# Optimization experiments

Measured on AMD Instinct MI355X. Metric: run time of the kernel, lower is better.

Reference implementation:

```python
import jax, jax.numpy as jnp
import numpy as np

N = 50000      # nodes
E = 500000     # edges
IN = 128       # in_channels
HID = 64       # hidden_channels
OUT = 128      # out_channels
H = 4          # heads
NEG_SLOPE = 0.2


def _glorot(key, shape):
    fan_in, fan_out = shape[0], shape[-1]
    lim = np.sqrt(6.0 / (fan_in + fan_out))
    return jax.random.uniform(key, shape, jnp.float32, -lim, lim)


def setup_inputs() -> dict:
    key = jax.random.key(0)
    ks = jax.random.split(key, 12)
    return {
        "x": jax.random.normal(ks[0], (N, IN), jnp.float32),
        "edge_index": jax.random.randint(ks[1], (2, E), 0, N, jnp.int64),
        "edge_weight": jax.random.uniform(ks[2], (E,), jnp.float32),
        # layer 1: IN -> H*HID
        "W1": _glorot(ks[3], (IN, H * HID)),
        "b1": jnp.zeros((H * HID,), jnp.float32),
        "att1": _glorot(ks[4], (H, HID)),
        # layer 2: HID -> H*HID  (update() means over heads -> HID features)
        "W2": _glorot(ks[5], (HID, H * HID)),
        "b2": jnp.zeros((H * HID,), jnp.float32),
        "att2": _glorot(ks[6], (H, HID)),
        # layer 3: HID -> H*OUT
        "W3": _glorot(ks[7], (HID, H * OUT)),
        "b3": jnp.zeros((H * OUT,), jnp.float32),
        "att3": _glorot(ks[8], (H, OUT)),
    }


def _gat_layer(x, W, b, att, src, dst, edge_weight, out_dim):
    # lin + reshape to [N, H, D]
    h = (x @ W + b).reshape(-1, H, out_dim)
    xj = h[src]                                   # gather source feats [E,H,D]
    alpha = jnp.sum(xj * att[None], axis=-1)      # per-edge att score [E,H]
    alpha = jax.nn.leaky_relu(alpha, NEG_SLOPE)
    alpha = alpha * edge_weight[:, None]
    alpha = jax.nn.softmax(alpha, axis=1)         # softmax over HEADS (dim=1, as in source)
    msg = xj * alpha[:, :, None]                  # [E,H,D]
    aggr = jax.ops.segment_sum(msg, dst, num_segments=N)  # scatter-add [N,H,D]
    return aggr.mean(axis=1)                      # update(): mean over heads -> [N,D]


def reference(x, edge_index, edge_weight, W1, b1, att1, W2, b2, att2, W3, b3, att3):
    src, dst = edge_index[0], edge_index[1]
    h = _gat_layer(x, W1, b1, att1, src, dst, edge_weight, HID)
    h = jax.nn.relu(h)
    h = _gat_layer(h, W2, b2, att2, src, dst, edge_weight, HID)
    h = jax.nn.relu(h)
    return _gat_layer(h, W3, b3, att3, src, dst, edge_weight, OUT)
```

## Files before the change

kernel.cpp:

```cpp
#include <hip/hip_runtime.h>
#include <hip/hip_bf16.h>

#define NHEAD 4
#define NEG 0.2f

typedef __bf16 bf16x8 __attribute__((ext_vector_type(8)));
typedef __bf16 bf16x4 __attribute__((ext_vector_type(4)));
typedef float f32x4 __attribute__((ext_vector_type(4)));

__device__ __forceinline__ float blo(unsigned u) { return __uint_as_float(u << 16); }
__device__ __forceinline__ float bhi(unsigned u) { return __uint_as_float(u & 0xffff0000u); }
__device__ __forceinline__ unsigned short fbits(float f) {
    __bf16 h = (__bf16)f;
    return *(unsigned short*)&h;
}


__global__ __launch_bounds__(256) void hist_k(const int* __restrict__ dst,
                                              int* __restrict__ deg, int E) {
    int e = blockIdx.x * 256 + threadIdx.x;
    if (e < E) atomicAdd(&deg[dst[e]], 1);
}

__global__ __launch_bounds__(256) void partial_k(const int* __restrict__ deg,
                                                 int* __restrict__ bsum, int n) {
    int t = threadIdx.x;
    int base = blockIdx.x * 2048 + t * 8;
    int s = 0;
#pragma unroll
    for (int i = 0; i < 8; ++i) {
        int idx = base + i;
        if (idx < n) s += deg[idx];
    }
#pragma unroll
    for (int off = 32; off; off >>= 1) s += __shfl_down(s, off, 64);
    __shared__ int ws[4];
    if ((t & 63) == 0) ws[t >> 6] = s;
    __syncthreads();
    if (t == 0) bsum[blockIdx.x] = ws[0] + ws[1] + ws[2] + ws[3];
}

__global__ __launch_bounds__(256) void bscan_k(const int* __restrict__ bsum,
                                               int* __restrict__ boff, int nb) {
    __shared__ int sh[256];
    int t = threadIdx.x;
    int v = (t < nb) ? bsum[t] : 0;
    sh[t] = v;
    __syncthreads();
    for (int off = 1; off < 256; off <<= 1) {
        int u = (t >= off) ? sh[t - off] : 0;
        __syncthreads();
        sh[t] += u;
        __syncthreads();
    }
    if (t < nb) boff[t] = sh[t] - v;
}

__global__ __launch_bounds__(256) void rescan_k(const int* __restrict__ deg,
                                                const int* __restrict__ boff,
                                                int* __restrict__ rowptr,
                                                int* __restrict__ fill,
                                                int n, int total) {
    __shared__ int ts[256];
    int t = threadIdx.x;
    int base = blockIdx.x * 2048 + t * 8;
    int v[8];
    int s = 0;
#pragma unroll
    for (int i = 0; i < 8; ++i) {
        int idx = base + i;
        v[i] = (idx < n) ? deg[idx] : 0;
        s += v[i];
    }
    ts[t] = s;
    __syncthreads();
    for (int off = 1; off < 256; off <<= 1) {
        int u = (t >= off) ? ts[t - off] : 0;
        __syncthreads();
        ts[t] += u;
        __syncthreads();
    }
    int run = boff[blockIdx.x] + ts[t] - s;
#pragma unroll
    for (int i = 0; i < 8; ++i) {
        int idx = base + i;
        if (idx < n) {
            rowptr[idx] = run;
            fill[idx] = run;
            run += v[i];
        }
    }
    if (blockIdx.x == 0 && t == 0) rowptr[n] = total;
}

__global__ __launch_bounds__(256) void scatter_k(const int* __restrict__ src,
                                                 const int* __restrict__ dst,
                                                 const float* __restrict__ ew,
                                                 int* __restrict__ fill,
                                                 int* __restrict__ srcs,
                                                 float* __restrict__ wsrt, int E) {
    int e = blockIdx.x * 256 + threadIdx.x;
    if (e < E) {
        int d = dst[e];
        int p = atomicAdd(&fill[d], 1);
        srcs[p] = src[e];
        wsrt[p] = ew[e];
    }
}


__global__ __launch_bounds__(256) void prep_k(const float* __restrict__ W1, const float* __restrict__ att1, const float* __restrict__ b1,
                                              const float* __restrict__ W2, const float* __restrict__ att2, const float* __restrict__ b2,
                                              const float* __restrict__ W3, const float* __restrict__ att3, const float* __restrict__ b3,
                                              float* __restrict__ v1, float* __restrict__ v2, float* __restrict__ v3,
                                              float* __restrict__ c1, float* __restrict__ c2, float* __restrict__ c3) {
    int tid = blockIdx.x * 256 + threadIdx.x;
    if (tid < 512) {
        int h = tid >> 7, k = tid & 127;
        float p = 0.f;
        for (int d = 0; d < 64; ++d) p += W1[k * 256 + h * 64 + d] * att1[h * 64 + d];
        v1[h * 128 + k] = p;
    } else if (tid < 768) {
        int t = tid - 512, h = t >> 6, k = t & 63;
        float p = 0.f;
        for (int d = 0; d < 64; ++d) p += W2[k * 256 + h * 64 + d] * att2[h * 64 + d];
        v2[h * 64 + k] = p;
    } else if (tid < 1024) {
        int t = tid - 768, h = t >> 6, k = t & 63;
        float p = 0.f;
        for (int d = 0; d < 128; ++d) p += W3[k * 512 + h * 128 + d] * att3[h * 128 + d];
        v3[h * 64 + k] = p;
    } else if (tid < 1028) {
        int h = tid - 1024;
        float p = 0.f;
        for (int d = 0; d < 64; ++d) p += b1[h * 64 + d] * att1[h * 64 + d];
        c1[h] = p;
    } else if (tid < 1032) {
        int h = tid - 1028;
        float p = 0.f;
        for (int d = 0; d < 64; ++d) p += b2[h * 64 + d] * att2[h * 64 + d];
        c2[h] = p;
    } else if (tid < 1036) {
        int h = tid - 1032;
        float p = 0.f;
        for (int d = 0; d < 128; ++d) p += b3[h * 128 + d] * att3[h * 128 + d];
        c3[h] = p;
    }
}


__global__ __launch_bounds__(256) void wpack3_k(const float* __restrict__ W1,
                                                const float* __restrict__ W2,
                                                const float* __restrict__ W3,
                                                unsigned short* __restrict__ Ws1,
                                                unsigned short* __restrict__ Ws2,
                                                unsigned short* __restrict__ Ws3) {
    int tid = blockIdx.x * 256 + threadIdx.x;
    if (tid < 32768) {
        int d = tid >> 9, r = tid & 511, h = r >> 7, k = r & 127;
        Ws1[tid] = fbits(W1[k * 256 + h * 64 + d]);
    } else if (tid < 49152) {
        int t = tid - 32768;
        int d = t >> 8, r = t & 255, h = r >> 6, k = r & 63;
        Ws2[t] = fbits(W2[k * 256 + h * 64 + d]);
    } else if (tid < 81920) {
        int t = tid - 49152;
        int d = t >> 8, r = t & 255, h = r >> 6, k = r & 63;
        Ws3[t] = fbits(W3[k * 512 + h * 128 + d]);
    }
}


__global__ __launch_bounds__(256) void xpack_score_k(const float* __restrict__ x,
                                                     const float* __restrict__ v1,
                                                     const float* __restrict__ c1,
                                                     unsigned* __restrict__ xb,
                                                     float* __restrict__ s, int n) {
    int gt = blockIdx.x * 256 + threadIdx.x;
    int node = gt >> 6, lane = gt & 63;
    if (node >= n) return;
    float2 xv = ((const float2*)(x + (size_t)node * 128))[lane];
    xb[(size_t)node * 64 + lane] = (unsigned)fbits(xv.x) | ((unsigned)fbits(xv.y) << 16);
    int d0 = 2 * lane;
    float p0 = xv.x * v1[0 * 128 + d0] + xv.y * v1[0 * 128 + d0 + 1];
    float p1 = xv.x * v1[1 * 128 + d0] + xv.y * v1[1 * 128 + d0 + 1];
    float p2 = xv.x * v1[2 * 128 + d0] + xv.y * v1[2 * 128 + d0 + 1];
    float p3 = xv.x * v1[3 * 128 + d0] + xv.y * v1[3 * 128 + d0 + 1];
#pragma unroll
    for (int off = 32; off; off >>= 1) {
        p0 += __shfl_xor(p0, off, 64);
        p1 += __shfl_xor(p1, off, 64);
        p2 += __shfl_xor(p2, off, 64);
        p3 += __shfl_xor(p3, off, 64);
    }
    if (lane == 0)
        *(float4*)&s[(size_t)node * 4] = make_float4(p0 + c1[0], p1 + c1[1], p2 + c1[2], p3 + c1[3]);
}


__device__ __forceinline__ float4 edge_alpha(const float* __restrict__ s, int sn, float w) {
    float4 sv = *(const float4*)&s[(size_t)sn * 4];
    float a0 = (sv.x > 0.f ? sv.x : NEG * sv.x) * w;
    float a1 = (sv.y > 0.f ? sv.y : NEG * sv.y) * w;
    float a2 = (sv.z > 0.f ? sv.z : NEG * sv.z) * w;
    float a3 = (sv.w > 0.f ? sv.w : NEG * sv.w) * w;
    float m = fmaxf(fmaxf(a0, a1), fmaxf(a2, a3));
    float e0 = __expf(a0 - m), e1 = __expf(a1 - m);
    float e2 = __expf(a2 - m), e3 = __expf(a3 - m);
    float inv = 0.25f / (e0 + e1 + e2 + e3);
    return make_float4(e0 * inv, e1 * inv, e2 * inv, e3 * inv);
}


template <int K, int D, bool LAST>
__global__ __launch_bounds__(256, 4) void fused_k(const int* __restrict__ rowptr,
                                                  const int* __restrict__ srcs,
                                                  const float* __restrict__ wsrt,
                                                  const float* __restrict__ sprev,
                                                  const unsigned* __restrict__ xb,
                                                  const unsigned short* __restrict__ Ws,
                                                  const float* __restrict__ bias,
                                                  const float* __restrict__ vnext,
                                                  const float* __restrict__ cnext,
                                                  unsigned short* __restrict__ aout,
                                                  float* __restrict__ fout,
                                                  float* __restrict__ snext,
                                                  int n) {
    constexpr int HK = 4 * K;
    constexpr int KS = HK / 32;
    constexpr int NC = D / 16;
    constexpr int CW = NC / 4;
    constexpr int DW = K / 32;

    __shared__ __bf16 gh[16 * HK];
    __shared__ __bf16 gl[16 * HK];
    __shared__ float4 A_lds[16];
    __shared__ float4 sc_lds[4][16];

    int t = threadIdx.x;
    int r0 = blockIdx.x * 16;
    int n4 = t >> 4, sl = t & 15;
    int node = r0 + n4;

    float acc[4][2 * DW];
#pragma unroll
    for (int h = 0; h < 4; ++h)
#pragma unroll
        for (int j = 0; j < 2 * DW; ++j) acc[h][j] = 0.f;
    float4 aA = make_float4(0.f, 0.f, 0.f, 0.f);

    auto load_u = [&](int sn, unsigned* u) {
        if constexpr (DW == 4) {
            uint4 ta = ((const uint4*)xb)[(size_t)sn * 16 + sl];
            u[0] = ta.x; u[1] = ta.y; u[2] = ta.z; u[3] = ta.w;
        } else {
            uint2 ta = ((const uint2*)xb)[(size_t)sn * 16 + sl];
            u[0] = ta.x; u[1] = ta.y;
        }
    };
    auto accum = [&](float4 al, const unsigned* u) {
#pragma unroll
        for (int j = 0; j < DW; ++j) {
            float x0 = blo(u[j]), x1 = bhi(u[j]);
            acc[0][2 * j] += al.x * x0; acc[0][2 * j + 1] += al.x * x1;
            acc[1][2 * j] += al.y * x0; acc[1][2 * j + 1] += al.y * x1;
            acc[2][2 * j] += al.z * x0; acc[2][2 * j + 1] += al.z * x1;
            acc[3][2 * j] += al.w * x0; acc[3][2 * j + 1] += al.w * x1;
        }
        aA.x += al.x; aA.y += al.y; aA.z += al.z; aA.w += al.w;
    };

    if (node < n) {
        int beg = rowptr[node], end = rowptr[node + 1];
        int e = beg;
        for (; e + 3 < end; e += 4) {
            int sn0 = srcs[e], sn1 = srcs[e + 1], sn2 = srcs[e + 2], sn3 = srcs[e + 3];
            float w0 = wsrt[e], w1 = wsrt[e + 1], w2 = wsrt[e + 2], w3 = wsrt[e + 3];
            unsigned u0[DW], u1[DW], u2[DW], u3[DW];
            load_u(sn0, u0); load_u(sn1, u1); load_u(sn2, u2); load_u(sn3, u3);
            float4 al0 = edge_alpha(sprev, sn0, w0);
            float4 al1 = edge_alpha(sprev, sn1, w1);
            float4 al2 = edge_alpha(sprev, sn2, w2);
            float4 al3 = edge_alpha(sprev, sn3, w3);
            accum(al0, u0); accum(al1, u1); accum(al2, u2); accum(al3, u3);
        }
        for (; e < end; ++e) {
            int sn = srcs[e];
            unsigned u[DW];
            load_u(sn, u);
            float4 al = edge_alpha(sprev, sn, wsrt[e]);
            accum(al, u);
        }
    }

    {
        char* ghb = (char*)gh + (size_t)n4 * (HK * 2);
        char* glb = (char*)gl + (size_t)n4 * (HK * 2);
        int sw = (n4 & 7) << 4;
#pragma unroll
        for (int h = 0; h < 4; ++h) {
            if constexpr (DW == 4) {
                bf16x8 vh, vl;
#pragma unroll
                for (int j = 0; j < 8; ++j) {
                    __bf16 hi = (__bf16)acc[h][j];
                    vh[j] = hi;
                    vl[j] = (__bf16)(acc[h][j] - (float)hi);
                }
                int bo = (h * K + sl * 8) * 2;
                *(bf16x8*)(ghb + (bo ^ sw)) = vh;
                *(bf16x8*)(glb + (bo ^ sw)) = vl;
            } else {
                bf16x4 vh, vl;
#pragma unroll
                for (int j = 0; j < 4; ++j) {
                    __bf16 hi = (__bf16)acc[h][j];
                    vh[j] = hi;
                    vl[j] = (__bf16)(acc[h][j] - (float)hi);
                }
                int bo = (h * K + sl * 4) * 2;
                *(bf16x4*)(ghb + (bo ^ sw)) = vh;
                *(bf16x4*)(glb + (bo ^ sw)) = vl;
            }
        }
        if (sl == 0) A_lds[n4] = aA;
    }
    __syncthreads();

    int wid = t >> 6, lane = t & 63;
    int lrow = lane & 15, gq = lane >> 4;

    f32x4 acc2[CW];
#pragma unroll
    for (int cw = 0; cw < CW; ++cw)
#pragma unroll
        for (int r = 0; r < 4; ++r) acc2[cw][r] = 0.f;

    const __bf16* wsp = (const __bf16*)Ws;
    const char* ghr = (const char*)gh + (size_t)lrow * (HK * 2);
    const char* glr = (const char*)gl + (size_t)lrow * (HK * 2);
    int swr = (lrow & 7) << 4;
#pragma unroll
    for (int ks = 0; ks < KS; ++ks) {
        int bo = ks * 64 + gq * 16;
        bf16x8 fh = *(const bf16x8*)(ghr + (bo ^ swr));
        bf16x8 fl = *(const bf16x8*)(glr + (bo ^ swr));
#pragma unroll
        for (int cw = 0; cw < CW; ++cw) {
            int c = wid * CW + cw;
            bf16x8 bfr = *(const bf16x8*)(wsp + (size_t)(c * 16 + lrow) * HK + ks * 32 + gq * 8);
            acc2[cw] = __builtin_amdgcn_mfma_f32_16x16x32_bf16(fh, bfr, acc2[cw], 0, 0, 0);
            acc2[cw] = __builtin_amdgcn_mfma_f32_16x16x32_bf16(fl, bfr, acc2[cw], 0, 0, 0);
        }
    }

    float4 Ar[4];
#pragma unroll
    for (int r = 0; r < 4; ++r) Ar[r] = A_lds[gq * 4 + r];

    float sc[4][4];
#pragma unroll
    for (int h = 0; h < 4; ++h)
#pragma unroll
        for (int r = 0; r < 4; ++r) sc[h][r] = 0.f;

#pragma unroll
    for (int cw = 0; cw < CW; ++cw) {
        int col = (wid * CW + cw) * 16 + lrow;
        float bb0 = bias[0 * D + col], bb1 = bias[1 * D + col];
        float bb2 = bias[2 * D + col], bb3 = bias[3 * D + col];
        float vv0 = 0.f, vv1 = 0.f, vv2 = 0.f, vv3 = 0.f;
        if constexpr (!LAST) {
            vv0 = vnext[0 * D + col]; vv1 = vnext[1 * D + col];
            vv2 = vnext[2 * D + col]; vv3 = vnext[3 * D + col];
        }
#pragma unroll
        for (int r = 0; r < 4; ++r) {
            float val = acc2[cw][r] + Ar[r].x * bb0 + Ar[r].y * bb1 + Ar[r].z * bb2 + Ar[r].w * bb3;
            int row = r0 + gq * 4 + r;
            if constexpr (LAST) {
                if (row < n) fout[(size_t)row * D + col] = val;
            } else {
                val = fmaxf(val, 0.f);
                if (row < n) aout[(size_t)row * D + col] = fbits(val);
                sc[0][r] += val * vv0;
                sc[1][r] += val * vv1;
                sc[2][r] += val * vv2;
                sc[3][r] += val * vv3;
            }
        }
    }

    if constexpr (!LAST) {
#pragma unroll
        for (int m = 1; m < 16; m <<= 1) {
#pragma unroll
            for (int h = 0; h < 4; ++h)
#pragma unroll
                for (int r = 0; r < 4; ++r) sc[h][r] += __shfl_xor(sc[h][r], m, 64);
        }
        if (lrow < 4) {
            int r = lrow;
            sc_lds[wid][gq * 4 + r] = make_float4(sc[0][r], sc[1][r], sc[2][r], sc[3][r]);
        }
        __syncthreads();
        if (t < 16) {
            int row = r0 + t;
            if (row < n) {
                float4 s0 = sc_lds[0][t], s1 = sc_lds[1][t];
                float4 s2 = sc_lds[2][t], s3 = sc_lds[3][t];
                *(float4*)&snext[(size_t)row * 4] =
                    make_float4(s0.x + s1.x + s2.x + s3.x + cnext[0],
                                s0.y + s1.y + s2.y + s3.y + cnext[1],
                                s0.z + s1.z + s2.z + s3.z + cnext[2],
                                s0.w + s1.w + s2.w + s3.w + cnext[3]);
            }
        }
    }
}


extern "C" void kernel_launch(void* const* d_in, const int* in_sizes, int n_in,
                              void* d_out, int out_size, void* d_ws, size_t ws_size,
                              hipStream_t stream) {
    const float* x    = (const float*)d_in[0];
    const int*   ei   = (const int*)d_in[1];
    const float* ew   = (const float*)d_in[2];
    const float* W1   = (const float*)d_in[3];
    const float* b1   = (const float*)d_in[4];
    const float* att1 = (const float*)d_in[5];
    const float* W2   = (const float*)d_in[6];
    const float* b2   = (const float*)d_in[7];
    const float* att2 = (const float*)d_in[8];
    const float* W3   = (const float*)d_in[9];
    const float* b3   = (const float*)d_in[10];
    const float* att3 = (const float*)d_in[11];

    const int N = in_sizes[0] / 128;
    const int E = in_sizes[2];
    const int* src = ei;
    const int* dst = ei + E;

    char* wp = (char*)d_ws;
    auto alloc = [&](size_t bytes) -> void* {
        void* p = (void*)wp;
        wp += (bytes + 511) & ~(size_t)511;
        return p;
    };
    int*   deg    = (int*)alloc((size_t)N * 4);
    int*   rowptr = (int*)alloc((size_t)(N + 1) * 4);
    int*   fill   = (int*)alloc((size_t)N * 4);
    int*   bsum   = (int*)alloc(256 * 4);
    int*   boff   = (int*)alloc(256 * 4);
    int*   srcs   = (int*)alloc((size_t)E * 4);
    float* wsrt   = (float*)alloc((size_t)E * 4);
    unsigned* xb  = (unsigned*)alloc((size_t)N * 64 * 4);
    float* s      = (float*)alloc((size_t)N * 4 * 4);
    float* s2     = (float*)alloc((size_t)N * 4 * 4);
    unsigned short* a1 = (unsigned short*)alloc((size_t)N * 64 * 2);
    unsigned short* a2 = (unsigned short*)alloc((size_t)N * 64 * 2);
    float* v1 = (float*)alloc(512 * 4);
    float* v2 = (float*)alloc(256 * 4);
    float* v3 = (float*)alloc(256 * 4);
    float* c1 = (float*)alloc(16);
    float* c2 = (float*)alloc(16);
    float* c3 = (float*)alloc(16);
    unsigned short* Ws1 = (unsigned short*)alloc(32768 * 2);
    unsigned short* Ws2 = (unsigned short*)alloc(16384 * 2);
    unsigned short* Ws3 = (unsigned short*)alloc(32768 * 2);

    wpack3_k<<<320, 256, 0, stream>>>(W1, W2, W3, Ws1, Ws2, Ws3);
    prep_k<<<5, 256, 0, stream>>>(W1, att1, b1, W2, att2, b2, W3, att3, b3,
                                  v1, v2, v3, c1, c2, c3);
    int gx = (N * 64 + 255) / 256;
    xpack_score_k<<<gx, 256, 0, stream>>>(x, v1, c1, xb, s, N);

    hipMemsetAsync(deg, 0, (size_t)N * 4, stream);
    int ge = (E + 255) / 256;
    int nb = (N + 2047) / 2048;
    hist_k<<<ge, 256, 0, stream>>>(dst, deg, E);
    partial_k<<<nb, 256, 0, stream>>>(deg, bsum, N);
    bscan_k<<<1, 256, 0, stream>>>(bsum, boff, nb);
    rescan_k<<<nb, 256, 0, stream>>>(deg, boff, rowptr, fill, N, E);
    scatter_k<<<ge, 256, 0, stream>>>(src, dst, ew, fill, srcs, wsrt, E);

    int gf = (N + 15) / 16;

    fused_k<128, 64, false><<<gf, 256, 0, stream>>>(rowptr, srcs, wsrt, s, xb, Ws1, b1,
                                                    v2, c2, a1, nullptr, s2, N);

    fused_k<64, 64, false><<<gf, 256, 0, stream>>>(rowptr, srcs, wsrt, s2, (const unsigned*)a1,
                                                   Ws2, b2, v3, c3, a2, nullptr, s, N);

    fused_k<64, 128, true><<<gf, 256, 0, stream>>>(rowptr, srcs, wsrt, s, (const unsigned*)a2,
                                                   Ws3, b3, nullptr, nullptr, nullptr,
                                                   (float*)d_out, nullptr, N);
}
```

Measured before the change: 257.1 us.

## Sort nodes by degree and precompute per-edge attention in separate kernel

Adds a counting sort of destination nodes by descending in-degree, so each 16-node block in the fused aggregation kernels handles nodes of similar degree, which reduces load imbalance and divergence within waves. CSR is built in permuted order and outputs are scattered back through the permutation. Per-edge softmax-over-heads alpha is moved out of the fused kernel into a separate alpha_k pass that writes an E×4 float buffer. This adds extra launches, an 8 MB alpha write/read per layer, and scattered output stores.

Result: slower. 571.6 us (+122.4%).

```diff
diff --git a/kernel.cpp b/kernel.cpp
--- a/kernel.cpp
+++ b/kernel.cpp
@@ -3,6 +3,7 @@
 
 #define NHEAD 4
 #define NEG 0.2f
+#define NB 512
 
 typedef __bf16 bf16x8 __attribute__((ext_vector_type(8)));
 typedef __bf16 bf16x4 __attribute__((ext_vector_type(4)));
@@ -20,6 +21,47 @@
                                               int* __restrict__ deg, int E) {
     int e = blockIdx.x * 256 + threadIdx.x;
     if (e < E) atomicAdd(&deg[dst[e]], 1);
+}
+
+__global__ __launch_bounds__(256) void dhist_k(const int* __restrict__ deg,
+                                               int* __restrict__ dcount, int n) {
+    int i = blockIdx.x * 256 + threadIdx.x;
+    if (i < n) {
+        int b = NB - 1 - min(deg[i], NB - 1);
+        atomicAdd(&dcount[b], 1);
+    }
+}
+
+__global__ __launch_bounds__(NB) void dscan_k(const int* __restrict__ dcount,
+                                              int* __restrict__ dbase) {
+    __shared__ int sh[NB];
+    int t = threadIdx.x;
+    int v = dcount[t];
+    sh[t] = v;
+    __syncthreads();
+    for (int off = 1; off < NB; off <<= 1) {
+        int u = (t >= off) ? sh[t - off] : 0;
+        __syncthreads();
+        sh[t] += u;
+        __syncthreads();
+    }
+    dbase[t] = sh[t] - v;
+}
+
+__global__ __launch_bounds__(256) void dscatter_k(const int* __restrict__ deg,
+                                                  int* __restrict__ dbase,
+                                                  int* __restrict__ perm,
+                                                  int* __restrict__ iperm,
+                                                  int* __restrict__ degp, int n) {
+    int i = blockIdx.x * 256 + threadIdx.x;
+    if (i < n) {
+        int d = deg[i];
+        int b = NB - 1 - min(d, NB - 1);
+        int pos = atomicAdd(&dbase[b], 1);
+        perm[pos] = i;
+        iperm[i] = pos;
+        degp[pos] = d;
+    }
 }
 
 __global__ __launch_bounds__(256) void partial_k(const int* __restrict__ deg,
@@ -96,15 +138,16 @@
 __global__ __launch_bounds__(256) void scatter_k(const int* __restrict__ src,
                                                  const int* __restrict__ dst,
                                                  const float* __restrict__ ew,
+                                                 const int* __restrict__ iperm,
                                                  int* __restrict__ fill,
                                                  int* __restrict__ srcs,
                                                  float* __restrict__ wsrt, int E) {
     int e = blockIdx.x * 256 + threadIdx.x;
     if (e < E) {
-        int d = dst[e];
-        int p = atomicAdd(&fill[d], 1);
-        srcs[p] = src[e];
-        wsrt[p] = ew[e];
+        int p = iperm[dst[e]];
+        int slot = atomicAdd(&fill[p], 1);
+        srcs[slot] = src[e];
+        wsrt[slot] = ew[e];
     }
 }
 
@@ -198,8 +241,15 @@
 }
 
 
-__device__ __forceinline__ float4 edge_alpha(const float* __restrict__ s, int sn, float w) {
-    float4 sv = *(const float4*)&s[(size_t)sn * 4];
+__global__ __launch_bounds__(256) void alpha_k(const int* __restrict__ srcs,
+                                               const float* __restrict__ wsrt,
+                                               const float* __restrict__ s,
+                                               float* __restrict__ alpha, int E) {
+    int e = blockIdx.x * 256 + threadIdx.x;
+    if (e >= E) return;
+    int sn = srcs[e];
+    float w = wsrt[e];
+    float4 sv = *(const float4*)&s[(size_t)sn * NHEAD];
     float a0 = (sv.x > 0.f ? sv.x : NEG * sv.x) * w;
     float a1 = (sv.y > 0.f ? sv.y : NEG * sv.y) * w;
     float a2 = (sv.z > 0.f ? sv.z : NEG * sv.z) * w;
@@ -208,15 +258,15 @@
     float e0 = __expf(a0 - m), e1 = __expf(a1 - m);
     float e2 = __expf(a2 - m), e3 = __expf(a3 - m);
     float inv = 0.25f / (e0 + e1 + e2 + e3);
-    return make_float4(e0 * inv, e1 * inv, e2 * inv, e3 * inv);
+    *(float4*)&alpha[(size_t)e * 4] = make_float4(e0 * inv, e1 * inv, e2 * inv, e3 * inv);
 }
 
 
 template <int K, int D, bool LAST>
 __global__ __launch_bounds__(256, 4) void fused_k(const int* __restrict__ rowptr,
                                                   const int* __restrict__ srcs,
-                                                  const float* __restrict__ wsrt,
-                                                  const float* __restrict__ sprev,
+                                                  const float* __restrict__ alpha,
+                                                  const int* __restrict__ perm,
                                                   const unsigned* __restrict__ xb,
                                                   const unsigned short* __restrict__ Ws,
                                                   const float* __restrict__ bias,
@@ -236,11 +286,14 @@
     __shared__ __bf16 gl[16 * HK];
     __shared__ float4 A_lds[16];
     __shared__ float4 sc_lds[4][16];
+    __shared__ int perm_lds[16];
 
     int t = threadIdx.x;
     int r0 = blockIdx.x * 16;
     int n4 = t >> 4, sl = t & 15;
-    int node = r0 + n4;
+    int q = r0 + n4;
+
+    if (t < 16) perm_lds[t] = (r0 + t < n) ? perm[r0 + t] : 0;
 
     float acc[4][2 * DW];
 #pragma unroll
@@ -270,25 +323,24 @@
         aA.x += al.x; aA.y += al.y; aA.z += al.z; aA.w += al.w;
     };
 
-    if (node < n) {
-        int beg = rowptr[node], end = rowptr[node + 1];
+    if (q < n) {
+        int beg = rowptr[q], end = rowptr[q + 1];
         int e = beg;
         for (; e + 3 < end; e += 4) {
             int sn0 = srcs[e], sn1 = srcs[e + 1], sn2 = srcs[e + 2], sn3 = srcs[e + 3];
-            float w0 = wsrt[e], w1 = wsrt[e + 1], w2 = wsrt[e + 2], w3 = wsrt[e + 3];
             unsigned u0[DW], u1[DW], u2[DW], u3[DW];
             load_u(sn0, u0); load_u(sn1, u1); load_u(sn2, u2); load_u(sn3, u3);
-            float4 al0 = edge_alpha(sprev, sn0, w0);
-            float4 al1 = edge_alpha(sprev, sn1, w1);
-            float4 al2 = edge_alpha(sprev, sn2, w2);
-            float4 al3 = edge_alpha(sprev, sn3, w3);
+            float4 al0 = *(const float4*)&alpha[(size_t)e * 4];
+            float4 al1 = *(const float4*)&alpha[(size_t)(e + 1) * 4];
+            float4 al2 = *(const float4*)&alpha[(size_t)(e + 2) * 4];
+            float4 al3 = *(const float4*)&alpha[(size_t)(e + 3) * 4];
             accum(al0, u0); accum(al1, u1); accum(al2, u2); accum(al3, u3);
         }
         for (; e < end; ++e) {
             int sn = srcs[e];
             unsigned u[DW];
             load_u(sn, u);
-            float4 al = edge_alpha(sprev, sn, wsrt[e]);
+            float4 al = *(const float4*)&alpha[(size_t)e * 4];
             accum(al, u);
         }
     }
@@ -355,8 +407,12 @@
     }
 
     float4 Ar[4];
-#pragma unroll
-    for (int r = 0; r < 4; ++r) Ar[r] = A_lds[gq * 4 + r];
+    int orow[4];
+#pragma unroll
+    for (int r = 0; r < 4; ++r) {
+        Ar[r] = A_lds[gq * 4 + r];
+        orow[r] = perm_lds[gq * 4 + r];
+    }
 
     float sc[4][4];
 #pragma unroll
@@ -379,10 +435,10 @@
             float val = acc2[cw][r] + Ar[r].x * bb0 + Ar[r].y * bb1 + Ar[r].z * bb2 + Ar[r].w * bb3;
             int row = r0 + gq * 4 + r;
             if constexpr (LAST) {
-                if (row < n) fout[(size_t)row * D + col] = val;
+                if (row < n) fout[(size_t)orow[r] * D + col] = val;
             } else {
                 val = fmaxf(val, 0.f);
-                if (row < n) aout[(size_t)row * D + col] = fbits(val);
+                if (row < n) aout[(size_t)orow[r] * D + col] = fbits(val);
                 sc[0][r] += val * vv0;
                 sc[1][r] += val * vv1;
                 sc[2][r] += val * vv2;
@@ -409,7 +465,7 @@
             if (row < n) {
                 float4 s0 = sc_lds[0][t], s1 = sc_lds[1][t];
                 float4 s2 = sc_lds[2][t], s3 = sc_lds[3][t];
-                *(float4*)&snext[(size_t)row * 4] =
+                *(float4*)&snext[(size_t)perm_lds[t] * 4] =
                     make_float4(s0.x + s1.x + s2.x + s3.x + cnext[0],
                                 s0.y + s1.y + s2.y + s3.y + cnext[1],
                                 s0.z + s1.z + s2.z + s3.z + cnext[2],
@@ -448,6 +504,11 @@
         return p;
     };
     int*   deg    = (int*)alloc((size_t)N * 4);
+    int*   degp   = (int*)alloc((size_t)N * 4);
+    int*   perm   = (int*)alloc((size_t)N * 4);
+    int*   iperm  = (int*)alloc((size_t)N * 4);
+    int*   dcount = (int*)alloc(NB * 4);
+    int*   dbase  = (int*)alloc(NB * 4);
     int*   rowptr = (int*)alloc((size_t)(N + 1) * 4);
     int*   fill   = (int*)alloc((size_t)N * 4);
     int*   bsum   = (int*)alloc(256 * 4);
@@ -457,6 +518,7 @@
     unsigned* xb  = (unsigned*)alloc((size_t)N * 64 * 4);
     float* s      = (float*)alloc((size_t)N * 4 * 4);
     float* s2     = (float*)alloc((size_t)N * 4 * 4);
+    float* alpha  = (float*)alloc((size_t)E * 4 * 4);
     unsigned short* a1 = (unsigned short*)alloc((size_t)N * 64 * 2);
     unsigned short* a2 = (unsigned short*)alloc((size_t)N * 64 * 2);
     float* v1 = (float*)alloc(512 * 4);
@@ -476,23 +538,31 @@
     xpack_score_k<<<gx, 256, 0, stream>>>(x, v1, c1, xb, s, N);
 
     hipMemsetAsync(deg, 0, (size_t)N * 4, stream);
+    hipMemsetAsync(dcount, 0, NB * 4, stream);
     int ge = (E + 255) / 256;
+    int gn = (N + 255) / 256;
     int nb = (N + 2047) / 2048;
     hist_k<<<ge, 256, 0, stream>>>(dst, deg, E);
-    partial_k<<<nb, 256, 0, stream>>>(deg, bsum, N);
+    dhist_k<<<gn, 256, 0, stream>>>(deg, dcount, N);
+    dscan_k<<<1, NB, 0, stream>>>(dcount, dbase);
+    dscatter_k<<<gn, 256, 0, stream>>>(deg, dbase, perm, iperm, degp, N);
+    partial_k<<<nb, 256, 0, stream>>>(degp, bsum, N);
     bscan_k<<<1, 256, 0, stream>>>(bsum, boff, nb);
-    rescan_k<<<nb, 256, 0, stream>>>(deg, boff, rowptr, fill, N, E);
-    scatter_k<<<ge, 256, 0, stream>>>(src, dst, ew, fill, srcs, wsrt, E);
+    rescan_k<<<nb, 256, 0, stream>>>(degp, boff, rowptr, fill, N, E);
+    scatter_k<<<ge, 256, 0, stream>>>(src, dst, ew, iperm, fill, srcs, wsrt, E);
 
     int gf = (N + 15) / 16;
 
-    fused_k<128, 64, false><<<gf, 256, 0, stream>>>(rowptr, srcs, wsrt, s, xb, Ws1, b1,
+    alpha_k<<<ge, 256, 0, stream>>>(srcs, wsrt, s, alpha, E);
+    fused_k<128, 64, false><<<gf, 256, 0, stream>>>(rowptr, srcs, alpha, perm, xb, Ws1, b1,
                                                     v2, c2, a1, nullptr, s2, N);
 
-    fused_k<64, 64, false><<<gf, 256, 0, stream>>>(rowptr, srcs, wsrt, s2, (const unsigned*)a1,
+    alpha_k<<<ge, 256, 0, stream>>>(srcs, wsrt, s2, alpha, E);
+    fused_k<64, 64, false><<<gf, 256, 0, stream>>>(rowptr, srcs, alpha, perm, (const unsigned*)a1,
                                                    Ws2, b2, v3, c3, a2, nullptr, s, N);
 
-    fused_k<64, 128, true><<<gf, 256, 0, stream>>>(rowptr, srcs, wsrt, s, (const unsigned*)a2,
+    alpha_k<<<ge, 256, 0, stream>>>(srcs, wsrt, s, alpha, E);
+    fused_k<64, 128, true><<<gf, 256, 0, stream>>>(rowptr, srcs, alpha, perm, (const unsigned*)a2,
                                                    Ws3, b3, nullptr, nullptr, nullptr,
                                                    (float*)d_out, nullptr, N);
 }
```

## Precompute per-edge attention in separate kernel and software-pipeline edge gathers

Applied to the files above, without the earlier changes.

Moves the per-edge leaky-relu/softmax-over-heads computation out of the fused aggregation kernel into a new alpha_k pass that writes a per-edge float4 array. The fused kernel then reads precomputed alpha instead of a gathered score plus weight. Its edge loop is restructured to prefetch the next group of four edges while accumulating the current group, with clamped indices and zeroed alpha for padding. This aims to hide gather latency and shorten the dependent chain in the hot loop, at the cost of three extra launches and an extra E×16-byte write and read per layer.

New measurement: 271.5 us. +5.6%, slower.

```diff
diff --git a/kernel.cpp b/kernel.cpp
--- a/kernel.cpp
+++ b/kernel.cpp
@@ -198,8 +198,15 @@
 }
 
 
-__device__ __forceinline__ float4 edge_alpha(const float* __restrict__ s, int sn, float w) {
-    float4 sv = *(const float4*)&s[(size_t)sn * 4];
+__global__ __launch_bounds__(256) void alpha_k(const int* __restrict__ srcs,
+                                               const float* __restrict__ wsrt,
+                                               const float* __restrict__ s,
+                                               float* __restrict__ alpha, int E) {
+    int e = blockIdx.x * 256 + threadIdx.x;
+    if (e >= E) return;
+    int sn = srcs[e];
+    float w = wsrt[e];
+    float4 sv = *(const float4*)&s[(size_t)sn * NHEAD];
     float a0 = (sv.x > 0.f ? sv.x : NEG * sv.x) * w;
     float a1 = (sv.y > 0.f ? sv.y : NEG * sv.y) * w;
     float a2 = (sv.z > 0.f ? sv.z : NEG * sv.z) * w;
@@ -208,15 +215,14 @@
     float e0 = __expf(a0 - m), e1 = __expf(a1 - m);
     float e2 = __expf(a2 - m), e3 = __expf(a3 - m);
     float inv = 0.25f / (e0 + e1 + e2 + e3);
-    return make_float4(e0 * inv, e1 * inv, e2 * inv, e3 * inv);
+    *(float4*)&alpha[(size_t)e * 4] = make_float4(e0 * inv, e1 * inv, e2 * inv, e3 * inv);
 }
 
 
 template <int K, int D, bool LAST>
 __global__ __launch_bounds__(256, 4) void fused_k(const int* __restrict__ rowptr,
                                                   const int* __restrict__ srcs,
-                                                  const float* __restrict__ wsrt,
-                                                  const float* __restrict__ sprev,
+                                                  const float* __restrict__ alpha,
                                                   const unsigned* __restrict__ xb,
                                                   const unsigned short* __restrict__ Ws,
                                                   const float* __restrict__ bias,
@@ -272,24 +278,41 @@
 
     if (node < n) {
         int beg = rowptr[node], end = rowptr[node + 1];
-        int e = beg;
-        for (; e + 3 < end; e += 4) {
-            int sn0 = srcs[e], sn1 = srcs[e + 1], sn2 = srcs[e + 2], sn3 = srcs[e + 3];
-            float w0 = wsrt[e], w1 = wsrt[e + 1], w2 = wsrt[e + 2], w3 = wsrt[e + 3];
-            unsigned u0[DW], u1[DW], u2[DW], u3[DW];
-            load_u(sn0, u0); load_u(sn1, u1); load_u(sn2, u2); load_u(sn3, u3);
-            float4 al0 = edge_alpha(sprev, sn0, w0);
-            float4 al1 = edge_alpha(sprev, sn1, w1);
-            float4 al2 = edge_alpha(sprev, sn2, w2);
-            float4 al3 = edge_alpha(sprev, sn3, w3);
-            accum(al0, u0); accum(al1, u1); accum(al2, u2); accum(al3, u3);
-        }
-        for (; e < end; ++e) {
-            int sn = srcs[e];
-            unsigned u[DW];
-            load_u(sn, u);
-            float4 al = edge_alpha(sprev, sn, wsrt[e]);
-            accum(al, u);
+        if (beg < end) {
+            int last = end - 1;
+            auto fetch = [&](int e, unsigned* u, float4& al) {
+                int idx = min(e, last);
+                load_u(srcs[idx], u);
+                float4 a = *(const float4*)&alpha[(size_t)idx * 4];
+                bool v = (e < end);
+                al = v ? a : make_float4(0.f, 0.f, 0.f, 0.f);
+            };
+            unsigned ua0[DW], ua1[DW], ua2[DW], ua3[DW];
+            float4 aa0, aa1, aa2, aa3;
+            fetch(beg + 0, ua0, aa0);
+            fetch(beg + 1, ua1, aa1);
+            fetch(beg + 2, ua2, aa2);
+            fetch(beg + 3, ua3, aa3);
+            for (int e = beg;;) {
+                int en = e + 4;
+                bool more = en < end;
+                unsigned ub0[DW], ub1[DW], ub2[DW], ub3[DW];
+                float4 ba0, ba1, ba2, ba3;
+                if (more) {
+                    fetch(en + 0, ub0, ba0);
+                    fetch(en + 1, ub1, ba1);
+                    fetch(en + 2, ub2, ba2);
+                    fetch(en + 3, ub3, ba3);
+                }
+                accum(aa0, ua0); accum(aa1, ua1); accum(aa2, ua2); accum(aa3, ua3);
+                if (!more) break;
+#pragma unroll
+                for (int j = 0; j < DW; ++j) {
+                    ua0[j] = ub0[j]; ua1[j] = ub1[j]; ua2[j] = ub2[j]; ua3[j] = ub3[j];
+                }
+                aa0 = ba0; aa1 = ba1; aa2 = ba2; aa3 = ba3;
+                e = en;
+            }
         }
     }
 
@@ -457,6 +480,7 @@
     unsigned* xb  = (unsigned*)alloc((size_t)N * 64 * 4);
     float* s      = (float*)alloc((size_t)N * 4 * 4);
     float* s2     = (float*)alloc((size_t)N * 4 * 4);
+    float* alpha  = (float*)alloc((size_t)E * 4 * 4);
     unsigned short* a1 = (unsigned short*)alloc((size_t)N * 64 * 2);
     unsigned short* a2 = (unsigned short*)alloc((size_t)N * 64 * 2);
     float* v1 = (float*)alloc(512 * 4);
@@ -486,13 +510,16 @@
 
     int gf = (N + 15) / 16;
 
-    fused_k<128, 64, false><<<gf, 256, 0, stream>>>(rowptr, srcs, wsrt, s, xb, Ws1, b1,
+    alpha_k<<<ge, 256, 0, stream>>>(srcs, wsrt, s, alpha, E);
+    fused_k<128, 64, false><<<gf, 256, 0, stream>>>(rowptr, srcs, alpha, xb, Ws1, b1,
                                                     v2, c2, a1, nullptr, s2, N);
 
-    fused_k<64, 64, false><<<gf, 256, 0, stream>>>(rowptr, srcs, wsrt, s2, (const unsigned*)a1,
+    alpha_k<<<ge, 256, 0, stream>>>(srcs, wsrt, s2, alpha, E);
+    fused_k<64, 64, false><<<gf, 256, 0, stream>>>(rowptr, srcs, alpha, (const unsigned*)a1,
                                                    Ws2, b2, v3, c3, a2, nullptr, s, N);
 
-    fused_k<64, 128, true><<<gf, 256, 0, stream>>>(rowptr, srcs, wsrt, s, (const unsigned*)a2,
+    alpha_k<<<ge, 256, 0, stream>>>(srcs, wsrt, s, alpha, E);
+    fused_k<64, 128, true><<<gf, 256, 0, stream>>>(rowptr, srcs, alpha, (const unsigned*)a2,
                                                    Ws3, b3, nullptr, nullptr, nullptr,
                                                    (float*)d_out, nullptr, N);
 }
```

## Precompute per-edge attention in separate kernel and halve LDS for split-bf16 GEMM

Applied to the files above, without the earlier changes.

Moves the per-edge leaky-relu/softmax-over-heads computation out of the fused aggregation kernels into a separate alpha_k launch per layer that writes a float4 per edge. The fused kernels then read contiguous alpha values instead of gathering node scores and recomputing the exponentials. The hi/lo bf16 split buffers in LDS are merged into one buffer used in two passes with extra barriers, to cut shared memory and raise occupancy. In exchange it adds three launches, an 8 MB alpha buffer written and read each layer, and serialised MFMA passes.

Result: slower. 291.3 us (+13.3%).

```diff
diff --git a/kernel.cpp b/kernel.cpp
--- a/kernel.cpp
+++ b/kernel.cpp
@@ -198,8 +198,15 @@
 }
 
 
-__device__ __forceinline__ float4 edge_alpha(const float* __restrict__ s, int sn, float w) {
-    float4 sv = *(const float4*)&s[(size_t)sn * 4];
+__global__ __launch_bounds__(256) void alpha_k(const int* __restrict__ srcs,
+                                               const float* __restrict__ wsrt,
+                                               const float* __restrict__ s,
+                                               float* __restrict__ alpha, int E) {
+    int e = blockIdx.x * 256 + threadIdx.x;
+    if (e >= E) return;
+    int sn = srcs[e];
+    float w = wsrt[e];
+    float4 sv = *(const float4*)&s[(size_t)sn * NHEAD];
     float a0 = (sv.x > 0.f ? sv.x : NEG * sv.x) * w;
     float a1 = (sv.y > 0.f ? sv.y : NEG * sv.y) * w;
     float a2 = (sv.z > 0.f ? sv.z : NEG * sv.z) * w;
@@ -208,15 +215,14 @@
     float e0 = __expf(a0 - m), e1 = __expf(a1 - m);
     float e2 = __expf(a2 - m), e3 = __expf(a3 - m);
     float inv = 0.25f / (e0 + e1 + e2 + e3);
-    return make_float4(e0 * inv, e1 * inv, e2 * inv, e3 * inv);
+    *(float4*)&alpha[(size_t)e * 4] = make_float4(e0 * inv, e1 * inv, e2 * inv, e3 * inv);
 }
 
 
 template <int K, int D, bool LAST>
 __global__ __launch_bounds__(256, 4) void fused_k(const int* __restrict__ rowptr,
                                                   const int* __restrict__ srcs,
-                                                  const float* __restrict__ wsrt,
-                                                  const float* __restrict__ sprev,
+                                                  const float* __restrict__ alpha,
                                                   const unsigned* __restrict__ xb,
                                                   const unsigned short* __restrict__ Ws,
                                                   const float* __restrict__ bias,
@@ -232,8 +238,7 @@
     constexpr int CW = NC / 4;
     constexpr int DW = K / 32;
 
-    __shared__ __bf16 gh[16 * HK];
-    __shared__ __bf16 gl[16 * HK];
+    __shared__ __bf16 g[16 * HK];
     __shared__ float4 A_lds[16];
     __shared__ float4 sc_lds[4][16];
 
@@ -275,84 +280,87 @@
         int e = beg;
         for (; e + 3 < end; e += 4) {
             int sn0 = srcs[e], sn1 = srcs[e + 1], sn2 = srcs[e + 2], sn3 = srcs[e + 3];
-            float w0 = wsrt[e], w1 = wsrt[e + 1], w2 = wsrt[e + 2], w3 = wsrt[e + 3];
             unsigned u0[DW], u1[DW], u2[DW], u3[DW];
             load_u(sn0, u0); load_u(sn1, u1); load_u(sn2, u2); load_u(sn3, u3);
-            float4 al0 = edge_alpha(sprev, sn0, w0);
-            float4 al1 = edge_alpha(sprev, sn1, w1);
-            float4 al2 = edge_alpha(sprev, sn2, w2);
-            float4 al3 = edge_alpha(sprev, sn3, w3);
+            float4 al0 = *(const float4*)&alpha[(size_t)e * 4];
+            float4 al1 = *(const float4*)&alpha[(size_t)(e + 1) * 4];
+            float4 al2 = *(const float4*)&alpha[(size_t)(e + 2) * 4];
+            float4 al3 = *(const float4*)&alpha[(size_t)(e + 3) * 4];
             accum(al0, u0); accum(al1, u1); accum(al2, u2); accum(al3, u3);
         }
         for (; e < end; ++e) {
             int sn = srcs[e];
             unsigned u[DW];
             load_u(sn, u);
-            float4 al = edge_alpha(sprev, sn, wsrt[e]);
+            float4 al = *(const float4*)&alpha[(size_t)e * 4];
             accum(al, u);
         }
     }
 
-    {
-        char* ghb = (char*)gh + (size_t)n4 * (HK * 2);
-        char* glb = (char*)gl + (size_t)n4 * (HK * 2);
+    int wid = t >> 6, lane = t & 63;
+    int lrow = lane & 15, gq = lane >> 4;
+
+    auto write_part = [&](bool lo) {
+        char* gb = (char*)g + (size_t)n4 * (HK * 2);
         int sw = (n4 & 7) << 4;
 #pragma unroll
         for (int h = 0; h < 4; ++h) {
             if constexpr (DW == 4) {
-                bf16x8 vh, vl;
+                bf16x8 v;
 #pragma unroll
                 for (int j = 0; j < 8; ++j) {
-                    __bf16 hi = (__bf16)acc[h][j];
-                    vh[j] = hi;
-                    vl[j] = (__bf16)(acc[h][j] - (float)hi);
+                    float a = acc[h][j];
+                    __bf16 hi = (__bf16)a;
+                    v[j] = lo ? (__bf16)(a - (float)hi) : hi;
                 }
                 int bo = (h * K + sl * 8) * 2;
-                *(bf16x8*)(ghb + (bo ^ sw)) = vh;
-                *(bf16x8*)(glb + (bo ^ sw)) = vl;
+                *(bf16x8*)(gb + (bo ^ sw)) = v;
             } else {
-                bf16x4 vh, vl;
+                bf16x4 v;
 #pragma unroll
                 for (int j = 0; j < 4; ++j) {
-                    __bf16 hi = (__bf16)acc[h][j];
-                    vh[j] = hi;
-                    vl[j] = (__bf16)(acc[h][j] - (float)hi);
+                    float a = acc[h][j];
+                    __bf16 hi = (__bf16)a;
+                    v[j] = lo ? (__bf16)(a - (float)hi) : hi;
                 }
                 int bo = (h * K + sl * 4) * 2;
-                *(bf16x4*)(ghb + (bo ^ sw)) = vh;
-                *(bf16x4*)(glb + (bo ^ sw)) = vl;
+                *(bf16x4*)(gb + (bo ^ sw)) = v;
             }
         }
-        if (sl == 0) A_lds[n4] = aA;
-    }
+    };
+
+    f32x4 acc2[CW];
+#pragma unroll
+    for (int cw = 0; cw < CW; ++cw)
+#pragma unroll
+        for (int r = 0; r < 4; ++r) acc2[cw][r] = 0.f;
+
+    const __bf16* wsp = (const __bf16*)Ws;
+    const char* gr = (const char*)g + (size_t)lrow * (HK * 2);
+    int swr = (lrow & 7) << 4;
+
+    auto mfma_pass = [&]() {
+#pragma unroll
+        for (int ks = 0; ks < KS; ++ks) {
+            int bo = ks * 64 + gq * 16;
+            bf16x8 fr = *(const bf16x8*)(gr + (bo ^ swr));
+#pragma unroll
+            for (int cw = 0; cw < CW; ++cw) {
+                int c = wid * CW + cw;
+                bf16x8 bfr = *(const bf16x8*)(wsp + (size_t)(c * 16 + lrow) * HK + ks * 32 + gq * 8);
+                acc2[cw] = __builtin_amdgcn_mfma_f32_16x16x32_bf16(fr, bfr, acc2[cw], 0, 0, 0);
+            }
+        }
+    };
+
+    write_part(false);
+    if (sl == 0) A_lds[n4] = aA;
     __syncthreads();
-
-    int wid = t >> 6, lane = t & 63;
-    int lrow = lane & 15, gq = lane >> 4;
-
-    f32x4 acc2[CW];
-#pragma unroll
-    for (int cw = 0; cw < CW; ++cw)
-#pragma unroll
-        for (int r = 0; r < 4; ++r) acc2[cw][r] = 0.f;
-
-    const __bf16* wsp = (const __bf16*)Ws;
-    const char* ghr = (const char*)gh + (size_t)lrow * (HK * 2);
-    const char* glr = (const char*)gl + (size_t)lrow * (HK * 2);
-    int swr = (lrow & 7) << 4;
-#pragma unroll
-    for (int ks = 0; ks < KS; ++ks) {
-        int bo = ks * 64 + gq * 16;
-        bf16x8 fh = *(const bf16x8*)(ghr + (bo ^ swr));
-        bf16x8 fl = *(const bf16x8*)(glr + (bo ^ swr));
-#pragma unroll
-        for (int cw = 0; cw < CW; ++cw) {
-            int c = wid * CW + cw;
-            bf16x8 bfr = *(const bf16x8*)(wsp + (size_t)(c * 16 + lrow) * HK + ks * 32 + gq * 8);
-            acc2[cw] = __builtin_amdgcn_mfma_f32_16x16x32_bf16(fh, bfr, acc2[cw], 0, 0, 0);
-            acc2[cw] = __builtin_amdgcn_mfma_f32_16x16x32_bf16(fl, bfr, acc2[cw], 0, 0, 0);
-        }
-    }
+    mfma_pass();
+    __syncthreads();
+    write_part(true);
+    __syncthreads();
+    mfma_pass();
 
     float4 Ar[4];
 #pragma unroll
@@ -457,6 +465,7 @@
     unsigned* xb  = (unsigned*)alloc((size_t)N * 64 * 4);
     float* s      = (float*)alloc((size_t)N * 4 * 4);
     float* s2     = (float*)alloc((size_t)N * 4 * 4);
+    float* alpha  = (float*)alloc((size_t)E * 4 * 4);
     unsigned short* a1 = (unsigned short*)alloc((size_t)N * 64 * 2);
     unsigned short* a2 = (unsigned short*)alloc((size_t)N * 64 * 2);
     float* v1 = (float*)alloc(512 * 4);
@@ -486,13 +495,16 @@
 
     int gf = (N + 15) / 16;
 
-    fused_k<128, 64, false><<<gf, 256, 0, stream>>>(rowptr, srcs, wsrt, s, xb, Ws1, b1,
+    alpha_k<<<ge, 256, 0, stream>>>(srcs, wsrt, s, alpha, E);
+    fused_k<128, 64, false><<<gf, 256, 0, stream>>>(rowptr, srcs, alpha, xb, Ws1, b1,
                                                     v2, c2, a1, nullptr, s2, N);
 
-    fused_k<64, 64, false><<<gf, 256, 0, stream>>>(rowptr, srcs, wsrt, s2, (const unsigned*)a1,
+    alpha_k<<<ge, 256, 0, stream>>>(srcs, wsrt, s2, alpha, E);
+    fused_k<64, 64, false><<<gf, 256, 0, stream>>>(rowptr, srcs, alpha, (const unsigned*)a1,
                                                    Ws2, b2, v3, c3, a2, nullptr, s, N);
 
-    fused_k<64, 128, true><<<gf, 256, 0, stream>>>(rowptr, srcs, wsrt, s, (const unsigned*)a2,
+    alpha_k<<<ge, 256, 0, stream>>>(srcs, wsrt, s, alpha, E);
+    fused_k<64, 128, true><<<gf, 256, 0, stream>>>(rowptr, srcs, alpha, (const unsigned*)a2,
                                                    Ws3, b3, nullptr, nullptr, nullptr,
                                                    (float*)d_out, nullptr, N);
 }
```
